# Kernel optimization log

Measured on AMD Instinct MI355X. Metric: run time of the kernel, lower is better.

Reference implementation:

```python
import jax, jax.numpy as jnp
from jax import lax
import numpy as np

BLOCKS = 6
DIM = 768
D_STATE = 16
D_CONV = 4
EXPAND = 2
HEADDIM = 64
D_INNER = EXPAND * DIM              # 1536
NHEADS = D_INNER // HEADDIM        # 24
CONV_DIM = D_INNER + 2 * D_STATE   # 1568 (ngroups=1)
D_IN_PROJ = 2 * D_INNER + 2 * D_STATE + NHEADS  # 3128
NPITCH = 128


def setup_inputs() -> dict:
    key = jax.random.key(0)
    ks = jax.random.split(key, 16)
    B, L = 4, 4096
    s = 0.02
    return {
        "x": jax.random.normal(ks[0], (B, L, DIM), jnp.float32),
        "type_IDs": jax.random.randint(ks[1], (B, L), 0, 2),
        "in_proj_w": jax.random.normal(ks[2], (BLOCKS, D_IN_PROJ, DIM), jnp.float32) * s,
        "conv_w": jax.random.normal(ks[3], (BLOCKS, CONV_DIM, D_CONV), jnp.float32) * 0.1,
        "conv_b": jnp.zeros((BLOCKS, CONV_DIM), jnp.float32),
        "dt_bias": jax.random.uniform(ks[4], (BLOCKS, NHEADS), jnp.float32, -4.0, -2.0),
        "A_log": jnp.tile(jnp.log(jnp.linspace(1.0, 16.0, NHEADS, dtype=jnp.float32)), (BLOCKS, 1)),
        "D": jnp.ones((BLOCKS, NHEADS), jnp.float32),
        "norm_w": jnp.ones((BLOCKS, D_INNER), jnp.float32),
        "out_proj_w": jax.random.normal(ks[5], (BLOCKS, DIM, D_INNER), jnp.float32) * s,
        "head_w": jax.random.normal(ks[6], (2, DIM, DIM), jnp.float32) * s,
        "head_b": jnp.zeros((2, DIM), jnp.float32),
        "head_out_w": jax.random.normal(ks[7], (2, 4, NPITCH, DIM), jnp.float32) * s,
        "head_out_b": jnp.zeros((2, 4, NPITCH), jnp.float32),
    }


def _mamba2_block(x, Wi, cw, cb, dtb, Alog, Dp, nw, Wo):
    B, L, _ = x.shape
    zxbcdt = jnp.einsum('bld,ed->ble', x, Wi)                 # [B,L,D_IN_PROJ]
    z = zxbcdt[..., :D_INNER]
    xBC = zxbcdt[..., D_INNER:D_INNER + CONV_DIM]
    dt = zxbcdt[..., -NHEADS:]
    # causal depthwise conv1d over time
    xc = jnp.pad(jnp.swapaxes(xBC, 1, 2), ((0, 0), (0, 0), (D_CONV - 1, 0)))
    xBC = lax.conv_general_dilated(xc, cw[:, None, :], (1,), 'VALID',
                                   feature_group_count=CONV_DIM,
                                   dimension_numbers=('NCH', 'OIH', 'NCH'))
    xBC = jax.nn.silu(jnp.swapaxes(xBC, 1, 2) + cb)            # [B,L,CONV_DIM]
    xs = xBC[..., :D_INNER].reshape(B, L, NHEADS, HEADDIM)
    Bm = xBC[..., D_INNER:D_INNER + D_STATE]                   # [B,L,N]
    Cm = xBC[..., D_INNER + D_STATE:]                          # [B,L,N]
    dt = jax.nn.softplus(dt + dtb)                             # [B,L,H]
    dA = jnp.exp(dt * (-jnp.exp(Alog)))                        # [B,L,H]
    dtx = dt[..., None] * xs                                   # [B,L,H,P]

    def step(h, inp):
        dA_t, dtx_t, B_t, C_t = inp
        h = h * dA_t[:, :, None, None] + dtx_t[..., None] * B_t[:, None, None, :]
        y = jnp.einsum('bhpn,bn->bhp', h, C_t)
        return h, y

    h0 = jnp.zeros((B, NHEADS, HEADDIM, D_STATE), x.dtype)
    mv = lambda a: jnp.moveaxis(a, 1, 0)
    _, ys = lax.scan(step, h0, (mv(dA), mv(dtx), mv(Bm), mv(Cm)))
    y = jnp.moveaxis(ys, 0, 1) + Dp[None, None, :, None] * xs   # [B,L,H,P]
    y = y.reshape(B, L, D_INNER) * jax.nn.silu(z)               # gated
    y = y * lax.rsqrt(jnp.mean(y * y, -1, keepdims=True) + 1e-5) * nw
    return jnp.einsum('bli,di->bld', y, Wo)


def _head(t, hw, hb, ow, ob):
    h = jnp.einsum('bld,ed->ble', t, hw) + hb
    velocity = jnp.einsum('bld,pd->blp', h, ow[0]) + ob[0]
    onset = jax.nn.sigmoid(jnp.einsum('bld,pd->blp', h, ow[1]) + ob[1])
    offset = jax.nn.sigmoid(jnp.einsum('bld,pd->blp', h, ow[2]) + ob[2])
    frames = jax.nn.sigmoid(jnp.einsum('bld,pd->blp', h, ow[3]) + ob[3])
    return velocity, frames, onset, offset


def reference(x, type_IDs, in_proj_w, conv_w, conv_b, dt_bias, A_log, D,
              norm_w, out_proj_w, head_w, head_b, head_out_w, head_out_b):
    for i in range(BLOCKS):
        x = _mamba2_block(x, in_proj_w[i], conv_w[i], conv_b[i], dt_bias[i],
                          A_log[i], D[i], norm_w[i], out_proj_w[i])
    cmask = (type_IDs == 0).astype(x.dtype)[..., None]
    fmask = (type_IDs == 1).astype(x.dtype)[..., None]
    cv, cf, con, coff = _head(x, head_w[0], head_b[0], head_out_w[0], head_out_b[0])
    fv, ff, fon, foff = _head(x, head_w[1], head_b[1], head_out_w[1], head_out_b[1])
    # masked (instead of ragged boolean gather) to stay jit-compatible
    return jnp.stack([cv * cmask, cf * cmask, con * cmask, coff * cmask,
                      fv * fmask, ff * fmask, fon * fmask, foff * fmask])
```

## Files before the change

kernel.cpp:

```cpp
#include <hip/hip_runtime.h>
#include <cstdint>
#include <cstddef>

#define L_SEQ   4096
#define BATCH   4
#define DIMM    768
#define D_INNER 1536
#define NHEADS  24
#define HEADDIM 64
#define D_STATE 16
#define CONVD   1568
#define D_IPROJ 3128
#define ZXP     3200
#define SEGLEN  64
#define NSEG    (L_SEQ / SEGLEN)

typedef _Float16 f16x8 __attribute__((ext_vector_type(8)));
typedef _Float16 f16x4 __attribute__((ext_vector_type(4)));
typedef float    f32x4 __attribute__((ext_vector_type(4)));

__device__ __forceinline__ void glds16(const _Float16* g, _Float16* l) {
  __builtin_amdgcn_global_load_lds(
      (__attribute__((address_space(1))) unsigned int*)g,
      (__attribute__((address_space(3))) unsigned int*)l, 16, 0, 0);
}

template <int OM>
__global__ __launch_bounds__(256, 2) void gemm_mfma(
    const _Float16* __restrict__ A, int lda,
    const _Float16* __restrict__ W,
    const float* __restrict__ bias,
    void* __restrict__ Cv, long ldc, long extra,
    int M, int N, int K,
    const int* __restrict__ tidsp, int thead)
{
  __shared__ __align__(16) char smem[33792];
  _Float16* As = (_Float16*)smem;
  _Float16* Ws = (_Float16*)(smem + 16384);
  const int tid = threadIdx.x;
  const int lane = tid & 63, wid = tid >> 6;
  const int wr = wid >> 1, wc = wid & 1;

  const int nbx = gridDim.x, nby = gridDim.y;
  const int flat = blockIdx.y * nbx + blockIdx.x;
  const int xcd = flat & 7;
  const int bidx = flat >> 3;
  const int rpx = nby >> 3;
  const int rl = bidx % rpx;
  const int ct = bidx / rpx;
  const long m0 = (long)(xcd * rpx + rl) * 128;
  const int n0 = ct * 128;

  const int la = lane & 15, lg = lane >> 4;
  const int srow = lane >> 3, schunk = lane & 7;

  f32x4 acc[4][4] = {};

  for (int k0 = 0; k0 < K; k0 += 64) {
    __syncthreads();
#pragma unroll
    for (int p = 0; p < 4; ++p) {
      const int rg = (wid << 2) + p;
      const int row = (rg << 3) + srow;
      const int scn = schunk ^ (row & 7);
      glds16(A + (m0 + row) * (long)lda + k0 + scn * 8, As + rg * 512);
      int n = n0 + row; if (n >= N) n = N - 1;
      glds16(W + (long)n * K + k0 + scn * 8, Ws + rg * 512);
    }
    asm volatile("s_waitcnt vmcnt(0)" ::: "memory");
    __syncthreads();
#pragma unroll
    for (int ks = 0; ks < 2; ++ks) {
      const int cc = ks * 4 + lg;
      f16x8 af[4], bfr[4];
#pragma unroll
      for (int i = 0; i < 4; ++i) {
        int ra = wr * 64 + i * 16 + la;
        int rb = wc * 64 + i * 16 + la;
        af[i]  = *(const f16x8*)&As[ra * 64 + ((cc ^ (ra & 7)) << 3)];
        bfr[i] = *(const f16x8*)&Ws[rb * 64 + ((cc ^ (rb & 7)) << 3)];
      }
#pragma unroll
      for (int i = 0; i < 4; ++i)
#pragma unroll
        for (int j = 0; j < 4; ++j)
          acc[i][j] = __builtin_amdgcn_mfma_f32_16x16x32_f16(af[i], bfr[j], acc[i][j], 0, 0, 0);
    }
  }

  float* epi = (float*)smem;
#pragma unroll
  for (int ph = 0; ph < 2; ++ph) {
    __syncthreads();
    if (wr == ph) {
#pragma unroll
      for (int i = 0; i < 4; ++i)
#pragma unroll
        for (int j = 0; j < 4; ++j)
#pragma unroll
          for (int r = 0; r < 4; ++r)
            epi[(i * 16 + lg * 4 + r) * 132 + wc * 64 + j * 16 + la] = acc[i][j][r];
    }
    __syncthreads();
    if (OM == 3) {
      const int q = n0 >> 7;
      const int rr = tid >> 5;
      const int ch = tid & 31;
#pragma unroll
      for (int ps = 0; ps < 8; ++ps) {
        int lrow = ps * 8 + rr;
        long gr = m0 + ph * 64 + lrow;
        float keep = (tidsp[gr] == thead) ? 1.f : 0.f;
        float4 v = *(float4*)&epi[lrow * 132 + ch * 4];
        float o[4] = {v.x, v.y, v.z, v.w};
#pragma unroll
        for (int e = 0; e < 4; ++e) {
          float vv = o[e] + bias[n0 + ch * 4 + e];
          if (q != 0) vv = 1.f / (1.f + expf(-vv));
          o[e] = vv * keep;
        }
        *(float4*)((float*)Cv + (long)q * extra + gr * 128 + ch * 4) =
            make_float4(o[0], o[1], o[2], o[3]);
      }
    } else {
      const int rr = tid >> 4;
      const int ch = tid & 15;
      const int col = n0 + ch * 8;
      float b[8] = {0.f, 0.f, 0.f, 0.f, 0.f, 0.f, 0.f, 0.f};
      if (OM == 2 && col < N) {
#pragma unroll
        for (int e = 0; e < 8; ++e) b[e] = bias[col + e];
      }
#pragma unroll
      for (int ps = 0; ps < 4; ++ps) {
        int lrow = ps * 16 + rr;
        long gr = m0 + ph * 64 + lrow;
        if (col < N) {
          float4 v0 = *(float4*)&epi[lrow * 132 + ch * 8];
          float4 v1 = *(float4*)&epi[lrow * 132 + ch * 8 + 4];
          f16x8 o = {(_Float16)(v0.x + b[0]), (_Float16)(v0.y + b[1]),
                     (_Float16)(v0.z + b[2]), (_Float16)(v0.w + b[3]),
                     (_Float16)(v1.x + b[4]), (_Float16)(v1.y + b[5]),
                     (_Float16)(v1.z + b[6]), (_Float16)(v1.w + b[7])};
          *(f16x8*)((_Float16*)Cv + gr * ldc + col) = o;
        }
      }
    }
  }
}

__global__ __launch_bounds__(256) void cvt_kernel(
    const float* __restrict__ src, _Float16* __restrict__ dst, long n4)
{
  long i = (long)blockIdx.x * 256 + threadIdx.x;
  long stride = (long)gridDim.x * 256;
  for (; i < n4; i += stride) {
    float4 v = *(const float4*)(src + i * 4);
    f16x4 o = { (_Float16)v.x, (_Float16)v.y, (_Float16)v.z, (_Float16)v.w };
    *(f16x4*)(dst + i * 4) = o;
  }
}

__global__ __launch_bounds__(256) void pack_head_kernel(
    const float* __restrict__ how, const float* __restrict__ hob,
    _Float16* __restrict__ howb, float* __restrict__ hobp)
{
  const int wmap[4] = {0, 3, 1, 2};
  int idx = blockIdx.x * 256 + threadIdx.x;
  if (idx < 2 * 512 * 768) {
    int t = idx / (512 * 768);
    int rem = idx - t * 512 * 768;
    int q = rem / (128 * 768);
    int rem2 = rem - q * 128 * 768;
    howb[idx] = (_Float16)how[((size_t)(t * 4 + wmap[q])) * 128 * 768 + rem2];
  }
  if (idx < 1024) {
    int t = idx >> 9, rem = idx & 511;
    int q = rem >> 7, pp = rem & 127;
    hobp[idx] = hob[(t * 4 + wmap[q]) * 128 + pp];
  }
}

__global__ __launch_bounds__(64) void scanA_kernel(
    const _Float16* __restrict__ zx, const float* __restrict__ cw,
    const float* __restrict__ cb, const float* __restrict__ dtb,
    const float* __restrict__ alog, const float* __restrict__ Dv,
    _Float16* __restrict__ ybuf, _Float16* __restrict__ bcbuf,
    float* __restrict__ Hseg, float* __restrict__ cumq)
{
  __shared__ _Float16 sbcr[67][32];
  __shared__ _Float16 sbc[SEGLEN][32];
  __shared__ float sdt[SEGLEN], sda[SEGLEN];
  const int lane = threadIdx.x;
  const int seg = blockIdx.x & (NSEG - 1);
  const int bh = blockIdx.x >> 6;
  const int h = bh % NHEADS, b = bh / NHEADS;
  const int bl0 = b * L_SEQ + seg * SEGLEN;

  for (int i = lane; i < 67 * 4; i += 64) {
    int r = i >> 2, q = (i & 3) << 3;
    f16x8 v = {};
    if (seg > 0 || r >= 3)
      v = *(const f16x8*)&zx[(size_t)(bl0 - 3 + r) * ZXP + 2 * D_INNER + q];
    *(f16x8*)&sbcr[r][q] = v;
  }
  {
    float raw = (float)zx[(size_t)(bl0 + lane) * ZXP + (D_INNER + CONVD) + h] + dtb[h];
    float sp = (raw > 20.f) ? raw : log1pf(expf(raw));
    sdt[lane] = sp;
    float da = expf(-expf(alog[h]) * sp);
    sda[lane] = da;
    float pp = da;
#pragma unroll
    for (int off = 1; off < 64; off <<= 1) {
      float tv = __shfl_up(pp, off, 64);
      if (lane >= off) pp *= tv;
    }
    cumq[(size_t)bh * L_SEQ + seg * SEGLEN + lane] = pp;
  }
  __syncthreads();

  for (int i = lane; i < SEGLEN * 32; i += 64) {
    int t = i >> 5, c = i & 31;
    float acc = cb[D_INNER + c];
#pragma unroll
    for (int k = 0; k < 4; ++k)
      acc = fmaf(cw[(D_INNER + c) * 4 + k], (float)sbcr[t + k][c], acc);
    float s = acc / (1.f + expf(-acc));
    _Float16 sh = (_Float16)s;
    sbc[t][c] = sh;
    bcbuf[(size_t)(bl0 + t) * 32 + c] = sh;
  }

  const int xc = h * HEADDIM + lane;
  const _Float16* xg = zx + (size_t)bl0 * ZXP + D_INNER + xc;
  const float cwx0 = cw[xc * 4 + 0], cwx1 = cw[xc * 4 + 1];
  const float cwx2 = cw[xc * 4 + 2], cwx3 = cw[xc * 4 + 3];
  const float cbx = cb[xc];
  const float Dh = Dv[h];
  float xw0 = 0.f, xw1 = 0.f, xw2 = 0.f;
  if (seg > 0) {
    xw0 = (float)xg[-3 * (long)ZXP];
    xw1 = (float)xg[-2 * (long)ZXP];
    xw2 = (float)xg[-1 * (long)ZXP];
  }
  float xcur = (float)xg[0];
  __syncthreads();

  float hs[16];
#pragma unroll
  for (int n = 0; n < 16; ++n) hs[n] = 0.f;

  _Float16* yg = ybuf + (size_t)bl0 * D_INNER + xc;
  for (int t = 0; t < SEGLEN; ++t) {
    float xnext = (t < SEGLEN - 1) ? (float)xg[(size_t)(t + 1) * ZXP] : 0.f;
    float xa = cbx;
    xa = fmaf(cwx0, xw0, xa);
    xa = fmaf(cwx1, xw1, xa);
    xa = fmaf(cwx2, xw2, xa);
    xa = fmaf(cwx3, xcur, xa);
    float xv = xa / (1.f + expf(-xa));
    float dav = sda[t];
    float coef = sdt[t] * xv;
    f16x8 bb0 = *(const f16x8*)&sbc[t][0];
    f16x8 bb1 = *(const f16x8*)&sbc[t][8];
    f16x8 cc0 = *(const f16x8*)&sbc[t][16];
    f16x8 cc1 = *(const f16x8*)&sbc[t][24];
    float y0 = 0.f, y1 = 0.f, y2 = 0.f, y3 = 0.f;
#pragma unroll
    for (int n = 0; n < 8; ++n) {
      float hv = fmaf(hs[n], dav, coef * (float)bb0[n]);
      hs[n] = hv;
      float cvv = (float)cc0[n];
      if ((n & 3) == 0)      y0 = fmaf(hv, cvv, y0);
      else if ((n & 3) == 1) y1 = fmaf(hv, cvv, y1);
      else if ((n & 3) == 2) y2 = fmaf(hv, cvv, y2);
      else                   y3 = fmaf(hv, cvv, y3);
    }
#pragma unroll
    for (int n = 0; n < 8; ++n) {
      float hv = fmaf(hs[8 + n], dav, coef * (float)bb1[n]);
      hs[8 + n] = hv;
      float cvv = (float)cc1[n];
      if ((n & 3) == 0)      y0 = fmaf(hv, cvv, y0);
      else if ((n & 3) == 1) y1 = fmaf(hv, cvv, y1);
      else if ((n & 3) == 2) y2 = fmaf(hv, cvv, y2);
      else                   y3 = fmaf(hv, cvv, y3);
    }
    yg[(size_t)t * D_INNER] = (_Float16)fmaf(Dh, xv, (y0 + y1) + (y2 + y3));
    xw0 = xw1; xw1 = xw2; xw2 = xcur; xcur = xnext;
  }

  float* Hst = Hseg + ((size_t)bh * NSEG + seg) * 1024 + lane * 16;
#pragma unroll
  for (int n = 0; n < 16; n += 4)
    *(float4*)&Hst[n] = make_float4(hs[n], hs[n + 1], hs[n + 2], hs[n + 3]);
}

__global__ __launch_bounds__(1024) void scanB_kernel(
    float* __restrict__ Hseg, const float* __restrict__ cumq)
{
  const int bh = blockIdx.x;
  const int t = threadIdx.x;
  __shared__ float sp[NSEG];
  if (t < NSEG) sp[t] = cumq[(size_t)bh * L_SEQ + t * SEGLEN + (SEGLEN - 1)];
  __syncthreads();
  float v[NSEG];
#pragma unroll
  for (int s = 0; s < NSEG; ++s)
    v[s] = Hseg[((size_t)bh * NSEG + s) * 1024 + t];
  float h = 0.f;
#pragma unroll
  for (int s = 0; s < NSEG; ++s) {
    Hseg[((size_t)bh * NSEG + s) * 1024 + t] = h;
    h = fmaf(sp[s], h, v[s]);
  }
}

__global__ __launch_bounds__(64) void scanC_kernel(
    _Float16* __restrict__ ybuf, const _Float16* __restrict__ bcbuf,
    const float* __restrict__ Hseg, const float* __restrict__ cumq)
{
  const int seg = blockIdx.x & (NSEG - 1);
  if (seg == 0) return;
  __shared__ float sc[SEGLEN][16];
  __shared__ float scq[SEGLEN];
  const int lane = threadIdx.x;
  const int bh = blockIdx.x >> 6;
  const int h = bh % NHEADS, b = bh / NHEADS;
  const int bl0 = b * L_SEQ + seg * SEGLEN;
  const float* slot = Hseg + ((size_t)bh * NSEG + seg) * 1024 + lane * 16;
  float hin[16];
#pragma unroll
  for (int n = 0; n < 16; n += 4) {
    float4 v = *(const float4*)(slot + n);
    hin[n] = v.x; hin[n + 1] = v.y; hin[n + 2] = v.z; hin[n + 3] = v.w;
  }
  for (int i = lane; i < SEGLEN * 2; i += 64) {
    int t = i >> 1, q = (i & 1) << 3;
    f16x8 v = *(const f16x8*)&bcbuf[(size_t)(bl0 + t) * 32 + D_STATE + q];
#pragma unroll
    for (int e = 0; e < 8; ++e) sc[t][q + e] = (float)v[e];
  }
  scq[lane] = cumq[(size_t)bh * L_SEQ + seg * SEGLEN + lane];
  __syncthreads();
  for (int t = 0; t < SEGLEN; ++t) {
    float dot = 0.f;
#pragma unroll
    for (int n = 0; n < 16; ++n) dot = fmaf(hin[n], sc[t][n], dot);
    size_t ad = (size_t)(bl0 + t) * D_INNER + h * HEADDIM + lane;
    ybuf[ad] = (_Float16)fmaf(scq[t], dot, (float)ybuf[ad]);
  }
}

__global__ __launch_bounds__(256) void norm_kernel(
    const _Float16* __restrict__ y, _Float16* __restrict__ zx,
    const float* __restrict__ nw)
{
  const int row = blockIdx.x;
  const int tid = threadIdx.x;
  const _Float16* yr = y + (size_t)row * D_INNER;
  _Float16* zr = zx + (size_t)row * ZXP;
  float v[6];
  float ss = 0.f;
#pragma unroll
  for (int jj = 0; jj < 6; ++jj) {
    int c = jj * 256 + tid;
    float yv = (float)yr[c];
    float zv = (float)zr[c];
    float sz = zv / (1.f + expf(-zv));
    float val = yv * sz;
    v[jj] = val;
    ss = fmaf(val, val, ss);
  }
#pragma unroll
  for (int off = 32; off > 0; off >>= 1) ss += __shfl_xor(ss, off, 64);
  __shared__ float red[4];
  if ((tid & 63) == 0) red[tid >> 6] = ss;
  __syncthreads();
  float tot = red[0] + red[1] + red[2] + red[3];
  float rs = rsqrtf(tot * (1.f / 1536.f) + 1e-5f);
#pragma unroll
  for (int jj = 0; jj < 6; ++jj) {
    int c = jj * 256 + tid;
    zr[c] = (_Float16)(v[jj] * rs * nw[c]);
  }
}

extern "C" void kernel_launch(void* const* d_in, const int* in_sizes, int n_in,
                              void* d_out, int out_size, void* d_ws, size_t ws_size,
                              hipStream_t stream)
{
  const float* x_in = (const float*)d_in[0];
  const int*   tids = (const int*)d_in[1];
  const float* ipw  = (const float*)d_in[2];
  const float* cw   = (const float*)d_in[3];
  const float* cb   = (const float*)d_in[4];
  const float* dtb  = (const float*)d_in[5];
  const float* alog = (const float*)d_in[6];
  const float* Dv   = (const float*)d_in[7];
  const float* nw   = (const float*)d_in[8];
  const float* opw  = (const float*)d_in[9];
  const float* hw   = (const float*)d_in[10];
  const float* hb   = (const float*)d_in[11];
  const float* how  = (const float*)d_in[12];
  const float* hob  = (const float*)d_in[13];
  float* out = (float*)d_out;

  char* p = (char*)d_ws;
  _Float16* ipw_b = (_Float16*)p; p += (size_t)14413824 * 2;
  _Float16* opw_b = (_Float16*)p; p += (size_t)7077888 * 2;
  _Float16* hw_b  = (_Float16*)p; p += (size_t)1179648 * 2;
  _Float16* how_b = (_Float16*)p; p += (size_t)786432 * 2;
  float*    hob_p = (float*)p;    p += (size_t)1024 * 4;
  const size_t used_w = (size_t)(p - (char*)d_ws);
  const size_t PB = 54528000;
  int nb = 4;
  while (nb > 1 && used_w + (size_t)nb * PB > ws_size) nb >>= 1;

  cvt_kernel<<<8192, 256, 0, stream>>>(ipw, ipw_b, 14413824 / 4);
  cvt_kernel<<<6912, 256, 0, stream>>>(opw, opw_b, 7077888 / 4);
  cvt_kernel<<<1152, 256, 0, stream>>>(hw, hw_b, 1179648 / 4);
  pack_head_kernel<<<3072, 256, 0, stream>>>(how, hob, how_b, hob_p);

  for (int b0 = 0; b0 < BATCH; b0 += nb) {
    const int MT = nb * L_SEQ;
    _Float16* zx    = (_Float16*)p;
    _Float16* ybuf  = zx + (size_t)MT * ZXP;
    _Float16* bcbuf = ybuf + (size_t)MT * D_INNER;
    float*    Hseg  = (float*)(bcbuf + (size_t)MT * 32);
    float*    cumq  = Hseg + (size_t)nb * NHEADS * NSEG * 1024;
    _Float16* xbuf  = (_Float16*)(cumq + (size_t)MT * NHEADS);
    _Float16* hbuf  = zx;

    cvt_kernel<<<6144, 256, 0, stream>>>(x_in + (size_t)b0 * L_SEQ * DIMM,
                                         xbuf, (long)MT * DIMM / 4);

    for (int i = 0; i < 6; ++i) {
      gemm_mfma<0><<<dim3((D_IPROJ + 127) / 128, MT / 128), 256, 0, stream>>>(
          xbuf, DIMM, ipw_b + (size_t)i * D_IPROJ * DIMM, nullptr,
          zx, ZXP, 0, MT, D_IPROJ, DIMM, nullptr, 0);
      scanA_kernel<<<nb * NHEADS * NSEG, 64, 0, stream>>>(
          zx, cw + (size_t)i * CONVD * 4, cb + i * CONVD,
          dtb + i * NHEADS, alog + i * NHEADS, Dv + i * NHEADS,
          ybuf, bcbuf, Hseg, cumq);
      scanB_kernel<<<nb * NHEADS, 1024, 0, stream>>>(Hseg, cumq);
      scanC_kernel<<<nb * NHEADS * NSEG, 64, 0, stream>>>(ybuf, bcbuf, Hseg, cumq);
      norm_kernel<<<MT, 256, 0, stream>>>(ybuf, zx, nw + i * D_INNER);
      gemm_mfma<0><<<dim3(DIMM / 128, MT / 128), 256, 0, stream>>>(
          zx, ZXP, opw_b + (size_t)i * DIMM * D_INNER, nullptr,
          xbuf, DIMM, 0, MT, DIMM, D_INNER, nullptr, 0);
    }

    for (int t = 0; t < 2; ++t) {
      gemm_mfma<2><<<dim3(DIMM / 128, MT / 128), 256, 0, stream>>>(
          xbuf, DIMM, hw_b + (size_t)t * DIMM * DIMM, hb + t * DIMM,
          hbuf, DIMM, 0, MT, DIMM, DIMM, nullptr, 0);
      gemm_mfma<3><<<dim3(4, MT / 128), 256, 0, stream>>>(
          hbuf, DIMM, how_b + (size_t)t * 512 * DIMM, hob_p + t * 512,
          out + (size_t)t * 4 * 16384 * 128 + (size_t)b0 * L_SEQ * 128,
          128, (long)16384 * 128, MT, 512, DIMM,
          tids + (size_t)b0 * L_SEQ, t);
    }
  }
}
```

Before: 2.090 ms.

## Replace sequential per-segment SSM scan with chunked SSD matrix form on MFMA

Rewrites the intra-segment scan as the Mamba2 SSD chunk formulation. It builds a masked, decay-weighted C·Bᵀ matrix with MFMA, multiplies it by dt·x to get the intra-chunk outputs, and computes the segment end state as a weighted xᵀB product, also on MFMA. The cross-segment correction in scanC becomes an MFMA of C against the incoming state instead of per-lane dot products. The aim is to remove the serial 64-step recurrence in favour of matrix-core work. In exchange it adds fp16 rounding of intermediates and state, more LDS traffic, and extra exp evaluations in the masking loop.

```diff
diff --git a/kernel.cpp b/kernel.cpp
--- a/kernel.cpp
+++ b/kernel.cpp
@@ -181,42 +181,49 @@
   }
 }
 
-__global__ __launch_bounds__(64) void scanA_kernel(
+__global__ __launch_bounds__(64) void ssdA_kernel(
     const _Float16* __restrict__ zx, const float* __restrict__ cw,
     const float* __restrict__ cb, const float* __restrict__ dtb,
     const float* __restrict__ alog, const float* __restrict__ Dv,
     _Float16* __restrict__ ybuf, _Float16* __restrict__ bcbuf,
     float* __restrict__ Hseg, float* __restrict__ cumq)
 {
-  __shared__ _Float16 sbcr[67][32];
-  __shared__ _Float16 sbc[SEGLEN][32];
-  __shared__ float sdt[SEGLEN], sda[SEGLEN];
+  __shared__ __align__(16) char sm[30720];
+  _Float16* Mr = (_Float16*)sm;
+  _Float16* XT = (_Float16*)(sm + 8192);
+  _Float16* XC = (_Float16*)(sm + 16384);
+  _Float16* BC = (_Float16*)(sm + 24832);
+  float* sdt = (float*)(sm + 29952);
+  float* sa  = (float*)(sm + 30208);
+  float* sw  = (float*)(sm + 30464);
   const int lane = threadIdx.x;
   const int seg = blockIdx.x & (NSEG - 1);
   const int bh = blockIdx.x >> 6;
   const int h = bh % NHEADS, b = bh / NHEADS;
   const int bl0 = b * L_SEQ + seg * SEGLEN;
 
+  _Float16* bcraw = Mr;
   for (int i = lane; i < 67 * 4; i += 64) {
     int r = i >> 2, q = (i & 3) << 3;
     f16x8 v = {};
     if (seg > 0 || r >= 3)
       v = *(const f16x8*)&zx[(size_t)(bl0 - 3 + r) * ZXP + 2 * D_INNER + q];
-    *(f16x8*)&sbcr[r][q] = v;
+    *(f16x8*)&bcraw[r * 32 + q] = v;
   }
   {
     float raw = (float)zx[(size_t)(bl0 + lane) * ZXP + (D_INNER + CONVD) + h] + dtb[h];
     float sp = (raw > 20.f) ? raw : log1pf(expf(raw));
     sdt[lane] = sp;
-    float da = expf(-expf(alog[h]) * sp);
-    sda[lane] = da;
-    float pp = da;
+    float av = expf(alog[h]) * sp;
 #pragma unroll
     for (int off = 1; off < 64; off <<= 1) {
-      float tv = __shfl_up(pp, off, 64);
-      if (lane >= off) pp *= tv;
-    }
-    cumq[(size_t)bh * L_SEQ + seg * SEGLEN + lane] = pp;
+      float tv = __shfl_up(av, off, 64);
+      if (lane >= off) av += tv;
+    }
+    sa[lane] = av;
+    cumq[(size_t)bh * L_SEQ + seg * SEGLEN + lane] = expf(-av);
+    float alast = __shfl(av, 63, 64);
+    sw[lane] = expf(av - alast);
   }
   __syncthreads();
 
@@ -225,19 +232,19 @@
     float acc = cb[D_INNER + c];
 #pragma unroll
     for (int k = 0; k < 4; ++k)
-      acc = fmaf(cw[(D_INNER + c) * 4 + k], (float)sbcr[t + k][c], acc);
+      acc = fmaf(cw[(D_INNER + c) * 4 + k], (float)bcraw[(t + k) * 32 + c], acc);
     float s = acc / (1.f + expf(-acc));
     _Float16 sh = (_Float16)s;
-    sbc[t][c] = sh;
+    BC[t * 40 + c] = sh;
     bcbuf[(size_t)(bl0 + t) * 32 + c] = sh;
   }
-
-  const int xc = h * HEADDIM + lane;
-  const _Float16* xg = zx + (size_t)bl0 * ZXP + D_INNER + xc;
-  const float cwx0 = cw[xc * 4 + 0], cwx1 = cw[xc * 4 + 1];
-  const float cwx2 = cw[xc * 4 + 2], cwx3 = cw[xc * 4 + 3];
-  const float cbx = cb[xc];
-  const float Dh = Dv[h];
+  __syncthreads();
+
+  const int xch = h * HEADDIM + lane;
+  const _Float16* xg = zx + (size_t)bl0 * ZXP + D_INNER + xch;
+  const float cwx0 = cw[xch * 4 + 0], cwx1 = cw[xch * 4 + 1];
+  const float cwx2 = cw[xch * 4 + 2], cwx3 = cw[xch * 4 + 3];
+  const float cbx = cb[xch];
   float xw0 = 0.f, xw1 = 0.f, xw2 = 0.f;
   if (seg > 0) {
     xw0 = (float)xg[-3 * (long)ZXP];
@@ -245,13 +252,6 @@
     xw2 = (float)xg[-1 * (long)ZXP];
   }
   float xcur = (float)xg[0];
-  __syncthreads();
-
-  float hs[16];
-#pragma unroll
-  for (int n = 0; n < 16; ++n) hs[n] = 0.f;
-
-  _Float16* yg = ybuf + (size_t)bl0 * D_INNER + xc;
   for (int t = 0; t < SEGLEN; ++t) {
     float xnext = (t < SEGLEN - 1) ? (float)xg[(size_t)(t + 1) * ZXP] : 0.f;
     float xa = cbx;
@@ -260,41 +260,109 @@
     xa = fmaf(cwx2, xw2, xa);
     xa = fmaf(cwx3, xcur, xa);
     float xv = xa / (1.f + expf(-xa));
-    float dav = sda[t];
-    float coef = sdt[t] * xv;
-    f16x8 bb0 = *(const f16x8*)&sbc[t][0];
-    f16x8 bb1 = *(const f16x8*)&sbc[t][8];
-    f16x8 cc0 = *(const f16x8*)&sbc[t][16];
-    f16x8 cc1 = *(const f16x8*)&sbc[t][24];
-    float y0 = 0.f, y1 = 0.f, y2 = 0.f, y3 = 0.f;
-#pragma unroll
-    for (int n = 0; n < 8; ++n) {
-      float hv = fmaf(hs[n], dav, coef * (float)bb0[n]);
-      hs[n] = hv;
-      float cvv = (float)cc0[n];
-      if ((n & 3) == 0)      y0 = fmaf(hv, cvv, y0);
-      else if ((n & 3) == 1) y1 = fmaf(hv, cvv, y1);
-      else if ((n & 3) == 2) y2 = fmaf(hv, cvv, y2);
-      else                   y3 = fmaf(hv, cvv, y3);
-    }
-#pragma unroll
-    for (int n = 0; n < 8; ++n) {
-      float hv = fmaf(hs[8 + n], dav, coef * (float)bb1[n]);
-      hs[8 + n] = hv;
-      float cvv = (float)cc1[n];
-      if ((n & 3) == 0)      y0 = fmaf(hv, cvv, y0);
-      else if ((n & 3) == 1) y1 = fmaf(hv, cvv, y1);
-      else if ((n & 3) == 2) y2 = fmaf(hv, cvv, y2);
-      else                   y3 = fmaf(hv, cvv, y3);
-    }
-    yg[(size_t)t * D_INNER] = (_Float16)fmaf(Dh, xv, (y0 + y1) + (y2 + y3));
+    XC[t * 66 + lane] = (_Float16)xv;
+    float dtx = sdt[t] * xv;
+    XT[lane * 64 + ((((t >> 3) ^ (lane & 7))) << 3) + (t & 7)] = (_Float16)dtx;
     xw0 = xw1; xw1 = xw2; xw2 = xcur; xcur = xnext;
   }
-
-  float* Hst = Hseg + ((size_t)bh * NSEG + seg) * 1024 + lane * 16;
-#pragma unroll
-  for (int n = 0; n < 16; n += 4)
-    *(float4*)&Hst[n] = make_float4(hs[n], hs[n + 1], hs[n + 2], hs[n + 3]);
+  __syncthreads();
+
+  const int la = lane & 15, lg = lane >> 4;
+
+  f32x4 acc1[4][4] = {};
+  {
+    f16x8 af[4], bf[4];
+#pragma unroll
+    for (int i = 0; i < 4; ++i) {
+      f16x8 v = {};
+      if (lg < 2) v = *(const f16x8*)&BC[(i * 16 + la) * 40 + 16 + lg * 8];
+      af[i] = v;
+    }
+#pragma unroll
+    for (int j = 0; j < 4; ++j) {
+      f16x8 v = {};
+      if (lg < 2) v = *(const f16x8*)&BC[(j * 16 + la) * 40 + lg * 8];
+      bf[j] = v;
+    }
+#pragma unroll
+    for (int i = 0; i < 4; ++i)
+#pragma unroll
+      for (int j = 0; j < 4; ++j)
+        acc1[i][j] = __builtin_amdgcn_mfma_f32_16x16x32_f16(af[i], bf[j], acc1[i][j], 0, 0, 0);
+  }
+#pragma unroll
+  for (int i = 0; i < 4; ++i)
+#pragma unroll
+    for (int j = 0; j < 4; ++j)
+#pragma unroll
+      for (int r = 0; r < 4; ++r) {
+        int t = i * 16 + lg * 4 + r, s = j * 16 + la;
+        float m = 0.f;
+        if (s <= t) m = acc1[i][j][r] * expf(sa[s] - sa[t]);
+        Mr[t * 64 + ((((s >> 3) ^ (t & 7))) << 3) + (s & 7)] = (_Float16)m;
+      }
+  __syncthreads();
+
+  f32x4 acc2[4][4] = {};
+#pragma unroll
+  for (int ks = 0; ks < 2; ++ks) {
+    const int cc = ks * 4 + lg;
+    f16x8 am[4], wx[4];
+#pragma unroll
+    for (int i = 0; i < 4; ++i) {
+      int rt = i * 16 + la;
+      am[i] = *(const f16x8*)&Mr[rt * 64 + ((cc ^ (rt & 7)) << 3)];
+    }
+#pragma unroll
+    for (int j = 0; j < 4; ++j) {
+      int rp = j * 16 + la;
+      wx[j] = *(const f16x8*)&XT[rp * 64 + ((cc ^ (rp & 7)) << 3)];
+    }
+#pragma unroll
+    for (int i = 0; i < 4; ++i)
+#pragma unroll
+      for (int j = 0; j < 4; ++j)
+        acc2[i][j] = __builtin_amdgcn_mfma_f32_16x16x32_f16(am[i], wx[j], acc2[i][j], 0, 0, 0);
+  }
+  const float Dh = Dv[h];
+#pragma unroll
+  for (int i = 0; i < 4; ++i)
+#pragma unroll
+    for (int j = 0; j < 4; ++j)
+#pragma unroll
+      for (int r = 0; r < 4; ++r) {
+        int t = i * 16 + lg * 4 + r, p = j * 16 + la;
+        float y = acc2[i][j][r] + Dh * (float)XC[t * 66 + p];
+        ybuf[(size_t)(bl0 + t) * D_INNER + h * HEADDIM + p] = (_Float16)y;
+      }
+
+  f32x4 acc3[4] = {};
+#pragma unroll
+  for (int ks = 0; ks < 2; ++ks) {
+    const int cc = ks * 4 + lg;
+    f16x8 b3;
+#pragma unroll
+    for (int e = 0; e < 8; ++e)
+      b3[e] = BC[(ks * 32 + lg * 8 + e) * 40 + la];
+#pragma unroll
+    for (int i = 0; i < 4; ++i) {
+      int rp = i * 16 + la;
+      f16x8 a3 = *(const f16x8*)&XT[rp * 64 + ((cc ^ (rp & 7)) << 3)];
+      f16x8 a3w;
+#pragma unroll
+      for (int e = 0; e < 8; ++e)
+        a3w[e] = (_Float16)((float)a3[e] * sw[ks * 32 + lg * 8 + e]);
+      acc3[i] = __builtin_amdgcn_mfma_f32_16x16x32_f16(a3w, b3, acc3[i], 0, 0, 0);
+    }
+  }
+  float* Hst = Hseg + ((size_t)bh * NSEG + seg) * 1024;
+#pragma unroll
+  for (int i = 0; i < 4; ++i)
+#pragma unroll
+    for (int r = 0; r < 4; ++r) {
+      int p = i * 16 + lg * 4 + r;
+      Hst[p * 16 + la] = acc3[i][r];
+    }
 }
 
 __global__ __launch_bounds__(1024) void scanB_kernel(
@@ -317,40 +385,56 @@
   }
 }
 
-__global__ __launch_bounds__(64) void scanC_kernel(
+__global__ __launch_bounds__(64) void ssdC_kernel(
     _Float16* __restrict__ ybuf, const _Float16* __restrict__ bcbuf,
     const float* __restrict__ Hseg, const float* __restrict__ cumq)
 {
   const int seg = blockIdx.x & (NSEG - 1);
   if (seg == 0) return;
-  __shared__ float sc[SEGLEN][16];
-  __shared__ float scq[SEGLEN];
   const int lane = threadIdx.x;
   const int bh = blockIdx.x >> 6;
   const int h = bh % NHEADS, b = bh / NHEADS;
   const int bl0 = b * L_SEQ + seg * SEGLEN;
-  const float* slot = Hseg + ((size_t)bh * NSEG + seg) * 1024 + lane * 16;
-  float hin[16];
-#pragma unroll
-  for (int n = 0; n < 16; n += 4) {
-    float4 v = *(const float4*)(slot + n);
-    hin[n] = v.x; hin[n + 1] = v.y; hin[n + 2] = v.z; hin[n + 3] = v.w;
-  }
-  for (int i = lane; i < SEGLEN * 2; i += 64) {
-    int t = i >> 1, q = (i & 1) << 3;
-    f16x8 v = *(const f16x8*)&bcbuf[(size_t)(bl0 + t) * 32 + D_STATE + q];
-#pragma unroll
-    for (int e = 0; e < 8; ++e) sc[t][q + e] = (float)v[e];
-  }
+  __shared__ float scq[SEGLEN];
   scq[lane] = cumq[(size_t)bh * L_SEQ + seg * SEGLEN + lane];
-  __syncthreads();
-  for (int t = 0; t < SEGLEN; ++t) {
-    float dot = 0.f;
-#pragma unroll
-    for (int n = 0; n < 16; ++n) dot = fmaf(hin[n], sc[t][n], dot);
-    size_t ad = (size_t)(bl0 + t) * D_INNER + h * HEADDIM + lane;
-    ybuf[ad] = (_Float16)fmaf(scq[t], dot, (float)ybuf[ad]);
-  }
+  const int la = lane & 15, lg = lane >> 4;
+  const float* slot = Hseg + ((size_t)bh * NSEG + seg) * 1024;
+
+  f16x8 a4[4], w4[4];
+#pragma unroll
+  for (int i = 0; i < 4; ++i) {
+    f16x8 v = {};
+    if (lg < 2)
+      v = *(const f16x8*)&bcbuf[(size_t)(bl0 + i * 16 + la) * 32 + 16 + lg * 8];
+    a4[i] = v;
+  }
+#pragma unroll
+  for (int j = 0; j < 4; ++j) {
+    f16x8 v = {};
+    if (lg < 2) {
+#pragma unroll
+      for (int e = 0; e < 8; ++e)
+        v[e] = (_Float16)slot[(j * 16 + la) * 16 + lg * 8 + e];
+    }
+    w4[j] = v;
+  }
+  f32x4 acc[4][4] = {};
+#pragma unroll
+  for (int i = 0; i < 4; ++i)
+#pragma unroll
+    for (int j = 0; j < 4; ++j)
+      acc[i][j] = __builtin_amdgcn_mfma_f32_16x16x32_f16(a4[i], w4[j], acc[i][j], 0, 0, 0);
+  __syncthreads();
+#pragma unroll
+  for (int i = 0; i < 4; ++i)
+#pragma unroll
+    for (int j = 0; j < 4; ++j)
+#pragma unroll
+      for (int r = 0; r < 4; ++r) {
+        int t = i * 16 + lg * 4 + r, p = j * 16 + la;
+        size_t ad = (size_t)(bl0 + t) * D_INNER + h * HEADDIM + p;
+        ybuf[ad] = (_Float16)((float)ybuf[ad] + scq[t] * acc[i][j][r]);
+      }
 }
 
 __global__ __launch_bounds__(256) void norm_kernel(
@@ -440,12 +524,12 @@
       gemm_mfma<0><<<dim3((D_IPROJ + 127) / 128, MT / 128), 256, 0, stream>>>(
           xbuf, DIMM, ipw_b + (size_t)i * D_IPROJ * DIMM, nullptr,
           zx, ZXP, 0, MT, D_IPROJ, DIMM, nullptr, 0);
-      scanA_kernel<<<nb * NHEADS * NSEG, 64, 0, stream>>>(
+      ssdA_kernel<<<nb * NHEADS * NSEG, 64, 0, stream>>>(
           zx, cw + (size_t)i * CONVD * 4, cb + i * CONVD,
           dtb + i * NHEADS, alog + i * NHEADS, Dv + i * NHEADS,
           ybuf, bcbuf, Hseg, cumq);
       scanB_kernel<<<nb * NHEADS, 1024, 0, stream>>>(Hseg, cumq);
-      scanC_kernel<<<nb * NHEADS * NSEG, 64, 0, stream>>>(ybuf, bcbuf, Hseg, cumq);
+      ssdC_kernel<<<nb * NHEADS * NSEG, 64, 0, stream>>>(ybuf, bcbuf, Hseg, cumq);
       norm_kernel<<<MT, 256, 0, stream>>>(ybuf, zx, nw + i * D_INNER);
       gemm_mfma<0><<<dim3(DIMM / 128, MT / 128), 256, 0, stream>>>(
           zx, ZXP, opw_b + (size_t)i * DIMM * D_INNER, nullptr,
```

New measurement: 2.110 ms. About the same (+1.0%).
